# Kernel tuning notes

Measured on AMD Instinct MI355X. Metric: run time of the kernel, lower is better.

Reference implementation:

```python
import jax, jax.numpy as jnp
import numpy as np
from jax import lax

N_SAMPLES1 = 128   # self.n_samples[0]
K = 64             # k in sample_and_group
RADIUS = 0.4       # self.radius[0]
BN_EPS = 1e-5
NEG_INF = -1e8
DIMS0 = [6, 64, 64, 128]      # mlps_in[0][0] -> mlps[0]
DIMS1 = [131, 128, 128, 512]  # 128+3 -> mlps[1] (use_light_weight=False)


def _fps(pos, n):
    # pos: (N,3) -> (n,) indices; deterministic start at point 0
    Np = pos.shape[0]
    def body(carry, _):
        dists, last = carry
        d = jnp.sum((pos - pos[last]) ** 2, axis=-1)
        dists = jnp.minimum(dists, d)
        return (dists, jnp.argmax(dists).astype(jnp.int32)), last
    _, idxs = lax.scan(body, (jnp.full((Np,), 1e10, pos.dtype), jnp.int32(0)), None, length=n)
    return idxs


def _gather(values, idx):
    # values (B,N,C), idx (B,...) -> (B,...,C)
    return jax.vmap(lambda v, i: v[i])(values, idx)


def _conv_bn_relu(x, W, b, g, be):
    # 1x1 Conv2d + BatchNorm2d (training-mode batch stats) + ReLU; x (B,n,k,Cin)
    y = jnp.einsum('bnkc,cd->bnkd', x, W) + b
    m = jnp.mean(y, axis=(0, 1, 2), keepdims=True)
    v = jnp.mean(jnp.square(y - m), axis=(0, 1, 2), keepdims=True)
    return jax.nn.relu((y - m) * lax.rsqrt(v + BN_EPS) * g + be)


def _forward(x, pos,
             W00, b00, g00, be00, W01, b01, g01, be01, W02, b02, g02, be02,
             W10, b10, g10, be10, W11, b11, g11, be11, W12, b12, g12, be12):
    # ---- stage 0: FPS + kNN grouping + conv-MLP + radius-masked max pool ----
    fidx = jax.vmap(lambda p: _fps(p, N_SAMPLES1))(pos)          # (B,128)
    sp = _gather(pos, fidx)                                      # (B,128,3) sampled_pos
    # squared pairwise distances (||a||^2+||b||^2-2ab); topk/mask on sq dist is
    # equivalent to topk/mask on sqrt dist (monotone), avoids sqrt(0) NaN grads
    sq = (jnp.sum(sp ** 2, -1)[:, :, None] + jnp.sum(pos ** 2, -1)[:, None, :]
          - 2.0 * jnp.einsum('bmd,bnd->bmn', sp, pos))           # (B,128,N)
    sq = jnp.maximum(sq, 0.0)
    neg, tidx = lax.top_k(-sq, K)                                # smallest-k
    topk_sq = -neg                                               # (B,128,64)
    gp = _gather(pos, tidx) - sp[:, :, None, :]                  # centered grouped pos
    gf = jnp.concatenate([gp, _gather(x, tidx)], axis=-1)        # (B,128,64,6)
    for (W, b, g, be) in ((W00, b00, g00, be00), (W01, b01, g01, be01), (W02, b02, g02, be02)):
        gf = _conv_bn_relu(gf, W, b, g, be)                      # (B,128,64,128)
    mask = topk_sq <= RADIUS * RADIUS
    x1 = jnp.max(jnp.where(mask[..., None], gf, NEG_INF), axis=2)  # (B,128,128)
    # ---- stage 1: global (n_samples == 1) ----
    g2 = jnp.concatenate([sp, x1], axis=-1)[:, None]             # (B,1,128,131)
    for (W, b, g, be) in ((W10, b10, g10, be10), (W11, b11, g11, be11), (W12, b12, g12, be12)):
        g2 = _conv_bn_relu(g2, W, b, g, be)                      # (B,1,128,512)
    global_x = jnp.max(g2[:, 0], axis=1, keepdims=True)          # (B,1,512)
    return global_x


def setup_inputs() -> dict:
    key = jax.random.key(0)
    ks = jax.random.split(key, 16)
    B, N = 16, 8192
    inp = {
        'x': jax.random.normal(ks[0], (B, N, 3), jnp.float32),
        'pos': jax.random.uniform(ks[1], (B, N, 3), jnp.float32),
    }
    ki = 2
    for li, dims in enumerate([DIMS0, DIMS1]):
        for ci in range(3):
            cin, cout = dims[ci], dims[ci + 1]
            inp[f'W{li}{ci}'] = jax.random.normal(ks[ki], (cin, cout), jnp.float32) * 0.05
            inp[f'b{li}{ci}'] = jnp.zeros((cout,), jnp.float32)
            inp[f'g{li}{ci}'] = jnp.ones((cout,), jnp.float32)
            inp[f'be{li}{ci}'] = jnp.zeros((cout,), jnp.float32)
            ki += 1
    return inp


def reference(x, pos,
              W00, b00, g00, be00, W01, b01, g01, be01, W02, b02, g02, be02,
              W10, b10, g10, be10, W11, b11, g11, be11, W12, b12, g12, be12):
    global_x = _forward(x, pos,
                        W00, b00, g00, be00, W01, b01, g01, be01, W02, b02, g02, be02,
                        W10, b10, g10, be10, W11, b11, g11, be11, W12, b12, g12, be12)
    pos_out = jnp.zeros((pos.shape[0], 1, 3), pos.dtype)
    return global_x, pos_out
```

## Files before the change

### kernel.cpp

```cpp
#include <hip/hip_runtime.h>
#include <cstdint>
#include <cstddef>

#define NPTS 8192
#define BATCH 16
#define MS 128
#define KNB 64
#define NBLK (BATCH * MS)


__device__ __forceinline__ float dpp_wave_max_f32(float v) {
  v = fmaxf(v, __int_as_float(__builtin_amdgcn_update_dpp((int)0xff800000, __float_as_int(v), 0x111, 0xf, 0xf, false)));
  v = fmaxf(v, __int_as_float(__builtin_amdgcn_update_dpp((int)0xff800000, __float_as_int(v), 0x112, 0xf, 0xf, false)));
  v = fmaxf(v, __int_as_float(__builtin_amdgcn_update_dpp((int)0xff800000, __float_as_int(v), 0x114, 0xf, 0xf, false)));
  v = fmaxf(v, __int_as_float(__builtin_amdgcn_update_dpp((int)0xff800000, __float_as_int(v), 0x118, 0xf, 0xf, false)));
  v = fmaxf(v, __int_as_float(__builtin_amdgcn_update_dpp((int)0xff800000, __float_as_int(v), 0x142, 0xa, 0xf, false)));
  v = fmaxf(v, __int_as_float(__builtin_amdgcn_update_dpp((int)0xff800000, __float_as_int(v), 0x143, 0xc, 0xf, false)));
  return v;
}

__device__ __forceinline__ float dpp_wave_min_f32(float v) {
  v = fminf(v, __int_as_float(__builtin_amdgcn_update_dpp(0x7f800000, __float_as_int(v), 0x111, 0xf, 0xf, false)));
  v = fminf(v, __int_as_float(__builtin_amdgcn_update_dpp(0x7f800000, __float_as_int(v), 0x112, 0xf, 0xf, false)));
  v = fminf(v, __int_as_float(__builtin_amdgcn_update_dpp(0x7f800000, __float_as_int(v), 0x114, 0xf, 0xf, false)));
  v = fminf(v, __int_as_float(__builtin_amdgcn_update_dpp(0x7f800000, __float_as_int(v), 0x118, 0xf, 0xf, false)));
  v = fminf(v, __int_as_float(__builtin_amdgcn_update_dpp(0x7f800000, __float_as_int(v), 0x142, 0xa, 0xf, false)));
  v = fminf(v, __int_as_float(__builtin_amdgcn_update_dpp(0x7f800000, __float_as_int(v), 0x143, 0xc, 0xf, false)));
  return v;
}

__device__ __forceinline__ unsigned dpp_wave_min_u32(unsigned v) {
  unsigned o;
  o = (unsigned)__builtin_amdgcn_update_dpp((int)0xffffffffu, (int)v, 0x111, 0xf, 0xf, false); v = (o < v) ? o : v;
  o = (unsigned)__builtin_amdgcn_update_dpp((int)0xffffffffu, (int)v, 0x112, 0xf, 0xf, false); v = (o < v) ? o : v;
  o = (unsigned)__builtin_amdgcn_update_dpp((int)0xffffffffu, (int)v, 0x114, 0xf, 0xf, false); v = (o < v) ? o : v;
  o = (unsigned)__builtin_amdgcn_update_dpp((int)0xffffffffu, (int)v, 0x118, 0xf, 0xf, false); v = (o < v) ? o : v;
  o = (unsigned)__builtin_amdgcn_update_dpp((int)0xffffffffu, (int)v, 0x142, 0xa, 0xf, false); v = (o < v) ? o : v;
  o = (unsigned)__builtin_amdgcn_update_dpp((int)0xffffffffu, (int)v, 0x143, 0xc, 0xf, false); v = (o < v) ? o : v;
  return v;
}

__device__ __forceinline__ float dpp_row_max_f32(float v) {
  v = fmaxf(v, __int_as_float(__builtin_amdgcn_update_dpp((int)0xff800000, __float_as_int(v), 0x111, 0xf, 0xf, false)));
  v = fmaxf(v, __int_as_float(__builtin_amdgcn_update_dpp((int)0xff800000, __float_as_int(v), 0x112, 0xf, 0xf, false)));
  v = fmaxf(v, __int_as_float(__builtin_amdgcn_update_dpp((int)0xff800000, __float_as_int(v), 0x114, 0xf, 0xf, false)));
  v = fmaxf(v, __int_as_float(__builtin_amdgcn_update_dpp((int)0xff800000, __float_as_int(v), 0x118, 0xf, 0xf, false)));
  return v;
}

__device__ __forceinline__ unsigned dpp_row_min_u32(unsigned v) {
  unsigned o;
  o = (unsigned)__builtin_amdgcn_update_dpp((int)0xffffffffu, (int)v, 0x111, 0xf, 0xf, false); v = (o < v) ? o : v;
  o = (unsigned)__builtin_amdgcn_update_dpp((int)0xffffffffu, (int)v, 0x112, 0xf, 0xf, false); v = (o < v) ? o : v;
  o = (unsigned)__builtin_amdgcn_update_dpp((int)0xffffffffu, (int)v, 0x114, 0xf, 0xf, false); v = (o < v) ? o : v;
  o = (unsigned)__builtin_amdgcn_update_dpp((int)0xffffffffu, (int)v, 0x118, 0xf, 0xf, false); v = (o < v) ? o : v;
  return v;
}

__device__ __forceinline__ float dpp_quad_min_f32(float v) {
  v = fminf(v, __int_as_float(__builtin_amdgcn_update_dpp(0x7f800000, __float_as_int(v), 0x111, 0xf, 0xf, false)));
  v = fminf(v, __int_as_float(__builtin_amdgcn_update_dpp(0x7f800000, __float_as_int(v), 0x112, 0xf, 0xf, false)));
  return v;
}

__device__ __forceinline__ unsigned dpp_quad_min_u32(unsigned v) {
  unsigned o;
  o = (unsigned)__builtin_amdgcn_update_dpp((int)0xffffffffu, (int)v, 0x111, 0xf, 0xf, false); v = (o < v) ? o : v;
  o = (unsigned)__builtin_amdgcn_update_dpp((int)0xffffffffu, (int)v, 0x112, 0xf, 0xf, false); v = (o < v) ? o : v;
  return v;
}

#define FPS_STEP(J)                                                        \
  {                                                                        \
    const int i = J * 1024 + t;                                            \
    const float dx = px[i] - lx;                                           \
    const float dy = py[i] - ly;                                           \
    const float dz = pz[i] - lz;                                           \
    const float d = dx * dx + dy * dy + dz * dz;                           \
    md##J = fminf(md##J, d);                                               \
  }

#define FPS_RESCAN(J)                                                      \
  if (md##J == wv) best = (unsigned)(J * 1024 + t);

__global__ __launch_bounds__(1024, 4) void fps_kernel(const float* __restrict__ pos,
                                                      float* __restrict__ sp) {
#pragma clang fp contract(off)
  extern __shared__ float smem[];
  float* px = smem;
  float* py = smem + NPTS;
  float* pz = smem + 2 * NPTS;
  __shared__ float wval[2][16];
  __shared__ unsigned widx[2][16];
  const int b = blockIdx.x;
  const float* P = pos + (size_t)b * NPTS * 3;
  const int t = threadIdx.x;
  const int wave = t >> 6;
  const int lane = t & 63;
  float md0 = 1e10f, md1 = 1e10f, md2 = 1e10f, md3 = 1e10f;
  float md4 = 1e10f, md5 = 1e10f, md6 = 1e10f, md7 = 1e10f;
  for (int i = t; i < NPTS; i += 1024) {
    px[i] = P[i * 3 + 0];
    py[i] = P[i * 3 + 1];
    pz[i] = P[i * 3 + 2];
  }
  float lx = P[0], ly = P[1], lz = P[2];
  __syncthreads();
  for (int it = 0; it < MS; ++it) {
    if (t == 0) {
      sp[((size_t)b * MS + it) * 3 + 0] = lx;
      sp[((size_t)b * MS + it) * 3 + 1] = ly;
      sp[((size_t)b * MS + it) * 3 + 2] = lz;
    }
    FPS_STEP(0) FPS_STEP(1) FPS_STEP(2) FPS_STEP(3)
    FPS_STEP(4) FPS_STEP(5) FPS_STEP(6) FPS_STEP(7)
    const float m01 = fmaxf(md0, md1), m23 = fmaxf(md2, md3);
    const float m45 = fmaxf(md4, md5), m67 = fmaxf(md6, md7);
    const float bv = fmaxf(fmaxf(m01, m23), fmaxf(m45, m67));
    const float wv = __int_as_float(
        __builtin_amdgcn_readlane(__float_as_int(dpp_wave_max_f32(bv)), 63));
    unsigned best = 0xffffffffu;
    if (bv == wv) {
      FPS_RESCAN(7) FPS_RESCAN(6) FPS_RESCAN(5) FPS_RESCAN(4)
      FPS_RESCAN(3) FPS_RESCAN(2) FPS_RESCAN(1) FPS_RESCAN(0)
    }
    const unsigned wi =
        (unsigned)__builtin_amdgcn_readlane((int)dpp_wave_min_u32(best), 63);
    const int par = it & 1;
    if (lane == 0) { wval[par][wave] = wv; widx[par][wave] = wi; }
    __syncthreads();
    const float a = wval[par][lane & 15];
    const float M = __int_as_float(
        __builtin_amdgcn_readlane(__float_as_int(dpp_row_max_f32(a)), 15));
    const unsigned c2 = (a == M) ? widx[par][lane & 15] : 0xffffffffu;
    const unsigned idx =
        (unsigned)__builtin_amdgcn_readlane((int)dpp_row_min_u32(c2), 15);
    lx = px[idx];
    ly = py[idx];
    lz = pz[idx];
  }
}

__global__ __launch_bounds__(256) void knn_kernel(const float* __restrict__ pos,
                                                  const float* __restrict__ xf,
                                                  const float* __restrict__ sp,
                                                  float* __restrict__ gf0,
                                                  float* __restrict__ sqsel) {
#pragma clang fp contract(off)
  __shared__ float sqv[NPTS];
  __shared__ float wval[2][4];
  __shared__ unsigned widx[2][4];
  __shared__ int sel_i[KNB];
  __shared__ float sel_v[KNB];
  const int bm = blockIdx.x;
  const int b = bm >> 7;
  const float* P = pos + (size_t)b * NPTS * 3;
  const float sx = sp[bm * 3 + 0], sy = sp[bm * 3 + 1], sz = sp[bm * 3 + 2];
  const float nsp = sx * sx + sy * sy + sz * sz;
  const int t = threadIdx.x;
  const int wave = t >> 6;
  const int lane = t & 63;
  for (int j = 0; j < 32; ++j) {
    const int i = j * 256 + t;
    const float qx = P[i * 3 + 0], qy = P[i * 3 + 1], qz = P[i * 3 + 2];
    const float npos = qx * qx + qy * qy + qz * qz;
    const float dt = sx * qx + sy * qy + sz * qz;
    float sq = (nsp + npos) - 2.0f * dt;
    sq = fmaxf(sq, 0.0f);
    sqv[i] = sq;
  }
  __syncthreads();
  float cv;
  unsigned ci;
  {
    unsigned long long k0 = ~0ULL;
    for (int j = 0; j < 32; ++j) {
      const int i = j * 256 + t;
      const unsigned long long key =
          ((unsigned long long)__float_as_uint(sqv[i]) << 32) | (unsigned)i;
      if (key < k0) k0 = key;
    }
    cv = __uint_as_float((unsigned)(k0 >> 32));
    ci = (unsigned)k0;
  }
  for (int round = 0; round < KNB; ++round) {
    const float wv = __int_as_float(
        __builtin_amdgcn_readlane(__float_as_int(dpp_wave_min_f32(cv)), 63));
    const unsigned sel = (cv == wv) ? ci : 0xffffffffu;
    const unsigned wi =
        (unsigned)__builtin_amdgcn_readlane((int)dpp_wave_min_u32(sel), 63);
    const int par = round & 1;
    if (lane == 0) { wval[par][wave] = wv; widx[par][wave] = wi; }
    __syncthreads();
    const float a = wval[par][lane & 3];
    const float M = __int_as_float(
        __builtin_amdgcn_readlane(__float_as_int(dpp_quad_min_f32(a)), 3));
    const unsigned c2 = (a == M) ? widx[par][lane & 3] : 0xffffffffu;
    const unsigned idx =
        (unsigned)__builtin_amdgcn_readlane((int)dpp_quad_min_u32(c2), 3);
    const int col = (int)(idx & 255u);
    if (t == col) {
      sel_i[round] = (int)idx;
      sel_v[round] = M;
      sqv[idx] = __uint_as_float(0x7f800000u);
    }
    if (wave == (col >> 6)) {
      float v = __uint_as_float(0x7f800000u);
      unsigned ii = 0xffffffffu;
      if (lane < 32) {
        const int i = lane * 256 + col;
        v = sqv[i];
        if (i == (int)idx) v = __uint_as_float(0x7f800000u);
        ii = (unsigned)i;
      }
      const float mv = __int_as_float(
          __builtin_amdgcn_readlane(__float_as_int(dpp_wave_min_f32(v)), 63));
      const unsigned s2 = (v == mv) ? ii : 0xffffffffu;
      const unsigned mi =
          (unsigned)__builtin_amdgcn_readlane((int)dpp_wave_min_u32(s2), 63);
      if (t == col) { cv = mv; ci = mi; }
    }
  }
  __syncthreads();
  if (t < KNB) {
    const int i = sel_i[t];
    const float* X = xf + (size_t)b * NPTS * 3;
    const size_t base = ((size_t)bm * KNB + t) * 6;
    gf0[base + 0] = P[i * 3 + 0] - sx;
    gf0[base + 1] = P[i * 3 + 1] - sy;
    gf0[base + 2] = P[i * 3 + 2] - sz;
    gf0[base + 3] = X[i * 3 + 0];
    gf0[base + 4] = X[i * 3 + 1];
    gf0[base + 5] = X[i * 3 + 2];
    sqsel[(size_t)bm * KNB + t] = sel_v[t];
  }
}

template <int MODE>
__global__ __launch_bounds__(256) void chain_kernel(
    const float* __restrict__ gf0,
    const float* __restrict__ W0, const float* __restrict__ B0,
    const float* __restrict__ W1, const float* __restrict__ B1,
    const float* __restrict__ W2, const float* __restrict__ B2,
    const float* __restrict__ sc1, const float* __restrict__ sh1,
    const float* __restrict__ sc2, const float* __restrict__ sh2,
    const float* __restrict__ sc3, const float* __restrict__ sh3,
    const float* __restrict__ sqsel,
    float* __restrict__ psum, float* __restrict__ psq, float* __restrict__ x1,
    float* __restrict__ z2out) {
  __shared__ float tA[64 * 65];
  __shared__ float tB[64 * 65];
  __shared__ float wbuf[64 * 64];
  __shared__ float in6[64 * 8];
  __shared__ float sqs[64];
  const int blk = blockIdx.x;
  const int t = threadIdx.x;
  {
    const float* G = gf0 + (size_t)blk * 64 * 6;
    for (int i = t; i < 384; i += 256) in6[(i / 6) * 8 + (i % 6)] = G[i];
    for (int i = t; i < 384; i += 256) wbuf[i] = W0[i];
    if (MODE == 4 && t < 64) sqs[t] = sqsel[(size_t)blk * 64 + t];
  }
  __syncthreads();
  const int r = t >> 2;
  const int c0 = (t & 3) * 16;
  float acc[16];
#pragma unroll
  for (int j = 0; j < 16; ++j) acc[j] = B0[c0 + j];
  for (int cin = 0; cin < 6; ++cin) {
    const float a = in6[r * 8 + cin];
#pragma unroll
    for (int j = 0; j < 16; ++j) acc[j] = fmaf(a, wbuf[cin * 64 + c0 + j], acc[j]);
  }
  if (MODE == 1) {
#pragma unroll
    for (int j = 0; j < 16; ++j) tA[r * 65 + c0 + j] = acc[j];
    __syncthreads();
    if (t < 64) {
      float s = 0.f, q = 0.f;
      for (int r2 = 0; r2 < 64; ++r2) { const float v = tA[r2 * 65 + t]; s += v; q += v * v; }
      psum[(size_t)t * NBLK + blk] = s;
      psq[(size_t)t * NBLK + blk] = q;
    }
    return;
  }
#pragma unroll
  for (int j = 0; j < 16; ++j) {
    const int c = c0 + j;
    tA[r * 65 + c] = fmaxf(fmaf(acc[j], sc1[c], sh1[c]), 0.f);
  }
  __syncthreads();
  for (int i = t; i < 4096; i += 256) wbuf[i] = W1[i];
  __syncthreads();
#pragma unroll
  for (int j = 0; j < 16; ++j) acc[j] = B1[c0 + j];
  for (int cin = 0; cin < 64; ++cin) {
    const float a = tA[r * 65 + cin];
    const float4* w4 = reinterpret_cast<const float4*>(&wbuf[cin * 64 + c0]);
#pragma unroll
    for (int k = 0; k < 4; ++k) {
      const float4 w = w4[k];
      acc[k * 4 + 0] = fmaf(a, w.x, acc[k * 4 + 0]);
      acc[k * 4 + 1] = fmaf(a, w.y, acc[k * 4 + 1]);
      acc[k * 4 + 2] = fmaf(a, w.z, acc[k * 4 + 2]);
      acc[k * 4 + 3] = fmaf(a, w.w, acc[k * 4 + 3]);
    }
  }
  if (MODE == 2) {
#pragma unroll
    for (int j = 0; j < 16; ++j) tB[r * 65 + c0 + j] = acc[j];
    __syncthreads();
    if (t < 64) {
      float s = 0.f, q = 0.f;
      for (int r2 = 0; r2 < 64; ++r2) { const float v = tB[r2 * 65 + t]; s += v; q += v * v; }
      psum[(size_t)t * NBLK + blk] = s;
      psq[(size_t)t * NBLK + blk] = q;
    }
    return;
  }
#pragma unroll
  for (int j = 0; j < 16; ++j) {
    const int c = c0 + j;
    tB[r * 65 + c] = fmaxf(fmaf(acc[j], sc2[c], sh2[c]), 0.f);
  }
  for (int hc = 0; hc < 2; ++hc) {
    __syncthreads();
    for (int i = t; i < 4096; i += 256) {
      const int cin = i >> 6, cc = i & 63;
      wbuf[i] = W2[cin * 128 + hc * 64 + cc];
    }
    if (MODE == 3 && hc == 0 && z2out != nullptr) {
      float* Zg = z2out + (size_t)blk * 4096;
      for (int i = t; i < 4096; i += 256) Zg[i] = tB[(i >> 6) * 65 + (i & 63)];
    }
    __syncthreads();
    float st_s = 0.f, st_q = 0.f, mx = -1e8f;
    for (int rh = 0; rh < 2; ++rh) {
      const int rr = rh * 32 + (t >> 3);
      const int cc0 = (t & 7) * 8;
      float a3[8];
#pragma unroll
      for (int j = 0; j < 8; ++j) a3[j] = B2[hc * 64 + cc0 + j];
      for (int cin = 0; cin < 64; ++cin) {
        const float a = tB[rr * 65 + cin];
        const float4* w4 = reinterpret_cast<const float4*>(&wbuf[cin * 64 + cc0]);
#pragma unroll
        for (int k = 0; k < 2; ++k) {
          const float4 w = w4[k];
          a3[k * 4 + 0] = fmaf(a, w.x, a3[k * 4 + 0]);
          a3[k * 4 + 1] = fmaf(a, w.y, a3[k * 4 + 1]);
          a3[k * 4 + 2] = fmaf(a, w.z, a3[k * 4 + 2]);
          a3[k * 4 + 3] = fmaf(a, w.w, a3[k * 4 + 3]);
        }
      }
      __syncthreads();
#pragma unroll
      for (int j = 0; j < 8; ++j) tA[(t >> 3) * 65 + cc0 + j] = a3[j];
      __syncthreads();
      if (t < 64) {
        if (MODE == 3) {
          for (int q2 = 0; q2 < 32; ++q2) { const float v = tA[q2 * 65 + t]; st_s += v; st_q += v * v; }
        } else {
          const float scv = sc3[hc * 64 + t], shv = sh3[hc * 64 + t];
          for (int q2 = 0; q2 < 32; ++q2) {
            const int kidx = rh * 32 + q2;
            const float y = tA[q2 * 65 + t];
            const float act = fmaxf(fmaf(y, scv, shv), 0.f);
            const float v = (sqs[kidx] <= 0.16f) ? act : -1e8f;
            mx = fmaxf(mx, v);
          }
        }
      }
      __syncthreads();
    }
    if (t < 64) {
      if (MODE == 3) {
        psum[(size_t)(hc * 64 + t) * NBLK + blk] = st_s;
        psq[(size_t)(hc * 64 + t) * NBLK + blk] = st_q;
      } else if (MODE == 4) {
        x1[(size_t)blk * 128 + hc * 64 + t] = mx;
      }
    }
  }
}

__global__ __launch_bounds__(256) void chain4c_kernel(
    const float* __restrict__ z2, const float* __restrict__ W2, const float* __restrict__ B2,
    const float* __restrict__ sc3, const float* __restrict__ sh3,
    const float* __restrict__ sqsel, float* __restrict__ x1) {
  __shared__ float tA[64 * 65];
  __shared__ float tB[64 * 65];
  __shared__ float wbuf[64 * 64];
  __shared__ float sqs[64];
  const int blk = blockIdx.x;
  const int t = threadIdx.x;
  const float* Zg = z2 + (size_t)blk * 4096;
  for (int i = t; i < 4096; i += 256) tB[(i >> 6) * 65 + (i & 63)] = Zg[i];
  if (t < 64) sqs[t] = sqsel[(size_t)blk * 64 + t];
  for (int hc = 0; hc < 2; ++hc) {
    __syncthreads();
    for (int i = t; i < 4096; i += 256) {
      const int cin = i >> 6, cc = i & 63;
      wbuf[i] = W2[cin * 128 + hc * 64 + cc];
    }
    __syncthreads();
    float mx = -1e8f;
    for (int rh = 0; rh < 2; ++rh) {
      const int rr = rh * 32 + (t >> 3);
      const int cc0 = (t & 7) * 8;
      float a3[8];
#pragma unroll
      for (int j = 0; j < 8; ++j) a3[j] = B2[hc * 64 + cc0 + j];
      for (int cin = 0; cin < 64; ++cin) {
        const float a = tB[rr * 65 + cin];
        const float4* w4 = reinterpret_cast<const float4*>(&wbuf[cin * 64 + cc0]);
#pragma unroll
        for (int k = 0; k < 2; ++k) {
          const float4 w = w4[k];
          a3[k * 4 + 0] = fmaf(a, w.x, a3[k * 4 + 0]);
          a3[k * 4 + 1] = fmaf(a, w.y, a3[k * 4 + 1]);
          a3[k * 4 + 2] = fmaf(a, w.z, a3[k * 4 + 2]);
          a3[k * 4 + 3] = fmaf(a, w.w, a3[k * 4 + 3]);
        }
      }
      __syncthreads();
#pragma unroll
      for (int j = 0; j < 8; ++j) tA[(t >> 3) * 65 + cc0 + j] = a3[j];
      __syncthreads();
      if (t < 64) {
        const float scv = sc3[hc * 64 + t], shv = sh3[hc * 64 + t];
        for (int q2 = 0; q2 < 32; ++q2) {
          const int kidx = rh * 32 + q2;
          const float y = tA[q2 * 65 + t];
          const float act = fmaxf(fmaf(y, scv, shv), 0.f);
          const float v = (sqs[kidx] <= 0.16f) ? act : -1e8f;
          mx = fmaxf(mx, v);
        }
      }
      __syncthreads();
    }
    if (t < 64) x1[(size_t)blk * 128 + hc * 64 + t] = mx;
  }
}

__global__ __launch_bounds__(256) void p_stats(const float* __restrict__ psum,
                                               const float* __restrict__ psq,
                                               float invN,
                                               const float* __restrict__ g,
                                               const float* __restrict__ be,
                                               float* __restrict__ sc,
                                               float* __restrict__ sh) {
  const int c = blockIdx.x;
  const int t = threadIdx.x;
  double s = 0.0, q = 0.0;
  for (int k = t; k < NBLK; k += 256) {
    s += (double)psum[(size_t)c * NBLK + k];
    q += (double)psq[(size_t)c * NBLK + k];
  }
  __shared__ double ss[256], qq[256];
  ss[t] = s;
  qq[t] = q;
  __syncthreads();
  for (int st = 128; st > 0; st >>= 1) {
    if (t < st) { ss[t] += ss[t + st]; qq[t] += qq[t + st]; }
    __syncthreads();
  }
  if (t == 0) {
    const double mean = ss[0] * (double)invN;
    double var = qq[0] * (double)invN - mean * mean;
    if (var < 0.0) var = 0.0;
    const float scl = (float)((double)g[c] / sqrt(var + 1e-5));
    sc[c] = scl;
    sh[c] = be[c] - (float)mean * scl;
  }
}

__global__ __launch_bounds__(128) void s1_kernel(const float* __restrict__ sp,
                                                 const float* __restrict__ x1,
                                                 const float* __restrict__ W,
                                                 const float* __restrict__ bia,
                                                 float* __restrict__ y1) {
  __shared__ float row[132];
  const int rowid = blockIdx.x;
  const int t = threadIdx.x;
  if (t < 3) row[t] = sp[(size_t)rowid * 3 + t];
  row[3 + t] = x1[(size_t)rowid * 128 + t];
  __syncthreads();
  float acc = bia[t];
  for (int cin = 0; cin < 131; ++cin) acc = fmaf(row[cin], W[(size_t)cin * 128 + t], acc);
  y1[(size_t)rowid * 128 + t] = acc;
}

__global__ __launch_bounds__(128) void s2_kernel(const float* __restrict__ y1,
                                                 const float* __restrict__ sc, const float* __restrict__ sh,
                                                 const float* __restrict__ W, const float* __restrict__ bia,
                                                 float* __restrict__ y2) {
  __shared__ float row[128];
  const int rowid = blockIdx.x;
  const int t = threadIdx.x;
  row[t] = fmaxf(fmaf(y1[(size_t)rowid * 128 + t], sc[t], sh[t]), 0.f);
  __syncthreads();
  float acc = bia[t];
  for (int cin = 0; cin < 128; ++cin) acc = fmaf(row[cin], W[(size_t)cin * 128 + t], acc);
  y2[(size_t)rowid * 128 + t] = acc;
}

__global__ __launch_bounds__(256) void s3_kernel(const float* __restrict__ y2,
                                                 const float* __restrict__ sc, const float* __restrict__ sh,
                                                 const float* __restrict__ W, const float* __restrict__ bia,
                                                 float* __restrict__ y3) {
  __shared__ float row[128];
  const int rowid = blockIdx.x;
  const int t = threadIdx.x;
  if (t < 128) row[t] = fmaxf(fmaf(y2[(size_t)rowid * 128 + t], sc[t], sh[t]), 0.f);
  __syncthreads();
  for (int h = 0; h < 2; ++h) {
    const int c = h * 256 + t;
    float acc = bia[c];
    for (int cin = 0; cin < 128; ++cin) acc = fmaf(row[cin], W[(size_t)cin * 512 + c], acc);
    y3[(size_t)rowid * 512 + c] = acc;
  }
}

__global__ __launch_bounds__(256) void s_stats(const float* __restrict__ y, int C, int rows,
                                               const float* __restrict__ g, const float* __restrict__ be,
                                               float* __restrict__ sc, float* __restrict__ sh) {
  const int c = blockIdx.x;
  const int t = threadIdx.x;
  double s = 0.0, q = 0.0;
  for (int r2 = t; r2 < rows; r2 += 256) {
    const double v = (double)y[(size_t)r2 * C + c];
    s += v;
    q += v * v;
  }
  __shared__ double ss[256], qq[256];
  ss[t] = s;
  qq[t] = q;
  __syncthreads();
  for (int st = 128; st > 0; st >>= 1) {
    if (t < st) { ss[t] += ss[t + st]; qq[t] += qq[t + st]; }
    __syncthreads();
  }
  if (t == 0) {
    const double mean = ss[0] / rows;
    double var = qq[0] / rows - mean * mean;
    if (var < 0.0) var = 0.0;
    const float scl = (float)((double)g[c] / sqrt(var + 1e-5));
    sc[c] = scl;
    sh[c] = be[c] - (float)mean * scl;
  }
}

__global__ __launch_bounds__(256) void final_kernel(const float* __restrict__ y3,
                                                    const float* __restrict__ sc, const float* __restrict__ sh,
                                                    float* __restrict__ out) {
  const int gid = blockIdx.x * 256 + threadIdx.x;
  const int b = gid >> 9;
  const int c = gid & 511;
  const float scv = sc[c], shv = sh[c];
  float mx = -3.402823466e+38f;
  for (int m = 0; m < 128; ++m) {
    const float v = fmaxf(fmaf(y3[((size_t)(b * 128 + m)) * 512 + c], scv, shv), 0.f);
    mx = fmaxf(mx, v);
  }
  out[gid] = mx;
  if (gid < 48) out[8192 + gid] = 0.f;
}

extern "C" void kernel_launch(void* const* d_in, const int* in_sizes, int n_in,
                              void* d_out, int out_size, void* d_ws, size_t ws_size,
                              hipStream_t stream) {
  const float* x    = (const float*)d_in[0];
  const float* pos  = (const float*)d_in[1];
  const float* W00  = (const float*)d_in[2];
  const float* b00  = (const float*)d_in[3];
  const float* g00  = (const float*)d_in[4];
  const float* be00 = (const float*)d_in[5];
  const float* W01  = (const float*)d_in[6];
  const float* b01  = (const float*)d_in[7];
  const float* g01  = (const float*)d_in[8];
  const float* be01 = (const float*)d_in[9];
  const float* W02  = (const float*)d_in[10];
  const float* b02  = (const float*)d_in[11];
  const float* g02  = (const float*)d_in[12];
  const float* be02 = (const float*)d_in[13];
  const float* W10  = (const float*)d_in[14];
  const float* b10  = (const float*)d_in[15];
  const float* g10  = (const float*)d_in[16];
  const float* be10 = (const float*)d_in[17];
  const float* W11  = (const float*)d_in[18];
  const float* b11  = (const float*)d_in[19];
  const float* g11  = (const float*)d_in[20];
  const float* be11 = (const float*)d_in[21];
  const float* W12  = (const float*)d_in[22];
  const float* b12  = (const float*)d_in[23];
  const float* g12  = (const float*)d_in[24];
  const float* be12 = (const float*)d_in[25];

  float* w = (float*)d_ws;
  float* sp    = w;
  float* gf0   = sp + 6144;
  float* sqsel = gf0 + 786432;
  float* x1    = sqsel + 131072;
  float* parts = x1 + 262144;
  float* psum  = parts;
  float* psq   = parts + 128 * NBLK;
  float* st    = parts + 524288;
  float* sc1 = st + 0,    *sh1 = st + 64;
  float* sc2 = st + 128,  *sh2 = st + 192;
  float* sc3 = st + 256,  *sh3 = st + 384;
  float* t1sc = st + 512, *t1sh = st + 640;
  float* t2sc = st + 768, *t2sh = st + 896;
  float* t3sc = st + 1024, *t3sh = st + 1536;
  float* y1s = st + 2048;
  float* y2s = y1s + 262144;
  float* y3s = y2s + 262144;
  const size_t Z2OFF = 3284992;
  const size_t Z2LEN = (size_t)NBLK * 4096;
  const bool cache_ok = ws_size >= (Z2OFF + Z2LEN) * sizeof(float);
  float* z2 = cache_ok ? (w + Z2OFF) : nullptr;

  fps_kernel<<<BATCH, 1024, 3 * NPTS * sizeof(float), stream>>>(pos, sp);
  knn_kernel<<<BATCH * MS, 256, 0, stream>>>(pos, x, sp, gf0, sqsel);

  const float invN0 = 1.0f / (float)(NBLK * KNB);
  chain_kernel<1><<<NBLK, 256, 0, stream>>>(gf0, W00, b00, W01, b01, W02, b02,
                                            sc1, sh1, sc2, sh2, sc3, sh3, sqsel, psum, psq, x1, nullptr);
  p_stats<<<64, 256, 0, stream>>>(psum, psq, invN0, g00, be00, sc1, sh1);
  chain_kernel<2><<<NBLK, 256, 0, stream>>>(gf0, W00, b00, W01, b01, W02, b02,
                                            sc1, sh1, sc2, sh2, sc3, sh3, sqsel, psum, psq, x1, nullptr);
  p_stats<<<64, 256, 0, stream>>>(psum, psq, invN0, g01, be01, sc2, sh2);
  chain_kernel<3><<<NBLK, 256, 0, stream>>>(gf0, W00, b00, W01, b01, W02, b02,
                                            sc1, sh1, sc2, sh2, sc3, sh3, sqsel, psum, psq, x1, z2);
  p_stats<<<128, 256, 0, stream>>>(psum, psq, invN0, g02, be02, sc3, sh3);
  if (cache_ok) {
    chain4c_kernel<<<NBLK, 256, 0, stream>>>(z2, W02, b02, sc3, sh3, sqsel, x1);
  } else {
    chain_kernel<4><<<NBLK, 256, 0, stream>>>(gf0, W00, b00, W01, b01, W02, b02,
                                              sc1, sh1, sc2, sh2, sc3, sh3, sqsel, psum, psq, x1, nullptr);
  }

  s1_kernel<<<NBLK, 128, 0, stream>>>(sp, x1, W10, b10, y1s);
  s_stats<<<128, 256, 0, stream>>>(y1s, 128, NBLK, g10, be10, t1sc, t1sh);
  s2_kernel<<<NBLK, 128, 0, stream>>>(y1s, t1sc, t1sh, W11, b11, y2s);
  s_stats<<<128, 256, 0, stream>>>(y2s, 128, NBLK, g11, be11, t2sc, t2sh);
  s3_kernel<<<NBLK, 256, 0, stream>>>(y2s, t2sc, t2sh, W12, b12, y3s);
  s_stats<<<512, 256, 0, stream>>>(y3s, 512, NBLK, g12, be12, t3sc, t3sh);
  final_kernel<<<32, 256, 0, stream>>>(y3s, t3sc, t3sh, (float*)d_out);
}
```

Before: 519.6 us.

## Materialize stage-0 MLP pre-activations per layer instead of recomputing chain

Replaces the recompute-the-whole-chain approach (each BN pass re-running all earlier layers) with per-layer kernels that store pre-activation outputs to workspace and reload them for the next layer. Layer 2/3 GEMMs use a 4x4 register tile with float4 shared-memory loads, and the final masked max pool becomes a light streaming kernel. This trades redundant FLOPs for extra global-memory traffic (about 32M floats written and read back) and needs a much larger workspace. It falls back to the old chain path when the workspace is too small.

After: 443.2 us. 14.7% less time.

```diff
diff --git a/kernel.cpp b/kernel.cpp
--- a/kernel.cpp
+++ b/kernel.cpp
@@ -7,7 +7,6 @@
 #define MS 128
 #define KNB 64
 #define NBLK (BATCH * MS)
-
 
 __device__ __forceinline__ float dpp_wave_max_f32(float v) {
   v = fmaxf(v, __int_as_float(__builtin_amdgcn_update_dpp((int)0xff800000, __float_as_int(v), 0x111, 0xf, 0xf, false)));
@@ -236,6 +235,191 @@
   }
 }
 
+
+__global__ __launch_bounds__(256) void l1_kernel(
+    const float* __restrict__ gf0, const float* __restrict__ W0,
+    const float* __restrict__ B0,
+    float* __restrict__ psum, float* __restrict__ psq,
+    float* __restrict__ y1pre) {
+  __shared__ float in6[64 * 8];
+  __shared__ float wbuf[384];
+  __shared__ float out[64 * 65];
+  const int blk = blockIdx.x;
+  const int t = threadIdx.x;
+  const float* G = gf0 + (size_t)blk * 384;
+  for (int i = t; i < 384; i += 256) in6[(i / 6) * 8 + (i % 6)] = G[i];
+  for (int i = t; i < 384; i += 256) wbuf[i] = W0[i];
+  __syncthreads();
+  const int r = t >> 2;
+  const int c0 = (t & 3) * 16;
+  float acc[16];
+#pragma unroll
+  for (int j = 0; j < 16; ++j) acc[j] = B0[c0 + j];
+  for (int cin = 0; cin < 6; ++cin) {
+    const float a = in6[r * 8 + cin];
+#pragma unroll
+    for (int j = 0; j < 16; ++j) acc[j] = fmaf(a, wbuf[cin * 64 + c0 + j], acc[j]);
+  }
+#pragma unroll
+  for (int j = 0; j < 16; ++j) out[r * 65 + c0 + j] = acc[j];
+  __syncthreads();
+  if (t < 64) {
+    float s = 0.f, q = 0.f;
+    for (int r2 = 0; r2 < 64; ++r2) { const float v = out[r2 * 65 + t]; s += v; q += v * v; }
+    psum[(size_t)t * NBLK + blk] = s;
+    psq[(size_t)t * NBLK + blk] = q;
+  }
+  float* Y = y1pre + (size_t)blk * 4096;
+  for (int i = t; i < 4096; i += 256) Y[i] = out[(i >> 6) * 65 + (i & 63)];
+}
+
+__global__ __launch_bounds__(256) void l2_kernel(
+    const float* __restrict__ ypre, const float* __restrict__ sc,
+    const float* __restrict__ sh, const float* __restrict__ W1,
+    const float* __restrict__ B1,
+    float* __restrict__ psum, float* __restrict__ psq,
+    float* __restrict__ yout) {
+  __shared__ float As[64 * 68];
+  __shared__ float Bs[64 * 64];
+  __shared__ float out[64 * 68];
+  const int blk = blockIdx.x;
+  const int t = threadIdx.x;
+  const float* Y = ypre + (size_t)blk * 4096;
+  for (int i = t; i < 4096; i += 256) {
+    const int c = i & 63;
+    As[(i >> 6) * 68 + c] = fmaxf(fmaf(Y[i], sc[c], sh[c]), 0.f);
+  }
+  for (int i = t; i < 4096; i += 256) Bs[i] = W1[i];
+  __syncthreads();
+  const int tr = t >> 4;
+  const int tc4 = (t & 15) * 4;
+  float acc[4][4];
+#pragma unroll
+  for (int s = 0; s < 4; ++s)
+#pragma unroll
+    for (int j = 0; j < 4; ++j) acc[s][j] = B1[tc4 + j];
+  for (int k0 = 0; k0 < 64; k0 += 4) {
+    float4 av[4];
+#pragma unroll
+    for (int s = 0; s < 4; ++s)
+      av[s] = *reinterpret_cast<const float4*>(&As[(tr + 16 * s) * 68 + k0]);
+#pragma unroll
+    for (int kk = 0; kk < 4; ++kk) {
+      const float4 bv = *reinterpret_cast<const float4*>(&Bs[(k0 + kk) * 64 + tc4]);
+#pragma unroll
+      for (int s = 0; s < 4; ++s) {
+        const float a = (kk == 0) ? av[s].x : (kk == 1) ? av[s].y
+                       : (kk == 2) ? av[s].z : av[s].w;
+        acc[s][0] = fmaf(a, bv.x, acc[s][0]);
+        acc[s][1] = fmaf(a, bv.y, acc[s][1]);
+        acc[s][2] = fmaf(a, bv.z, acc[s][2]);
+        acc[s][3] = fmaf(a, bv.w, acc[s][3]);
+      }
+    }
+  }
+#pragma unroll
+  for (int s = 0; s < 4; ++s) {
+    float4 o;
+    o.x = acc[s][0]; o.y = acc[s][1]; o.z = acc[s][2]; o.w = acc[s][3];
+    *reinterpret_cast<float4*>(&out[(tr + 16 * s) * 68 + tc4]) = o;
+  }
+  __syncthreads();
+  if (t < 64) {
+    float s = 0.f, q = 0.f;
+    for (int r2 = 0; r2 < 64; ++r2) { const float v = out[r2 * 68 + t]; s += v; q += v * v; }
+    psum[(size_t)t * NBLK + blk] = s;
+    psq[(size_t)t * NBLK + blk] = q;
+  }
+  float* O = yout + (size_t)blk * 4096;
+  for (int i = t; i < 4096; i += 256) O[i] = out[(i >> 6) * 68 + (i & 63)];
+}
+
+__global__ __launch_bounds__(256) void l3_kernel(
+    const float* __restrict__ ypre, const float* __restrict__ sc,
+    const float* __restrict__ sh, const float* __restrict__ W2,
+    const float* __restrict__ B2,
+    float* __restrict__ psum, float* __restrict__ psq,
+    float* __restrict__ yout) {
+  __shared__ float As[64 * 68];
+  __shared__ float Bs[64 * 64];
+  __shared__ float out[64 * 68];
+  const int blk = blockIdx.x;
+  const int t = threadIdx.x;
+  const float* Y = ypre + (size_t)blk * 4096;
+  for (int i = t; i < 4096; i += 256) {
+    const int c = i & 63;
+    As[(i >> 6) * 68 + c] = fmaxf(fmaf(Y[i], sc[c], sh[c]), 0.f);
+  }
+  const int tr = t >> 4;
+  const int tc4 = (t & 15) * 4;
+  for (int hc = 0; hc < 2; ++hc) {
+    __syncthreads();
+    for (int i = t; i < 4096; i += 256)
+      Bs[i] = W2[(i >> 6) * 128 + hc * 64 + (i & 63)];
+    __syncthreads();
+    float acc[4][4];
+#pragma unroll
+    for (int s = 0; s < 4; ++s)
+#pragma unroll
+      for (int j = 0; j < 4; ++j) acc[s][j] = B2[hc * 64 + tc4 + j];
+    for (int k0 = 0; k0 < 64; k0 += 4) {
+      float4 av[4];
+#pragma unroll
+      for (int s = 0; s < 4; ++s)
+        av[s] = *reinterpret_cast<const float4*>(&As[(tr + 16 * s) * 68 + k0]);
+#pragma unroll
+      for (int kk = 0; kk < 4; ++kk) {
+        const float4 bv = *reinterpret_cast<const float4*>(&Bs[(k0 + kk) * 64 + tc4]);
+#pragma unroll
+        for (int s = 0; s < 4; ++s) {
+          const float a = (kk == 0) ? av[s].x : (kk == 1) ? av[s].y
+                         : (kk == 2) ? av[s].z : av[s].w;
+          acc[s][0] = fmaf(a, bv.x, acc[s][0]);
+          acc[s][1] = fmaf(a, bv.y, acc[s][1]);
+          acc[s][2] = fmaf(a, bv.z, acc[s][2]);
+          acc[s][3] = fmaf(a, bv.w, acc[s][3]);
+        }
+      }
+    }
+#pragma unroll
+    for (int s = 0; s < 4; ++s) {
+      float4 o;
+      o.x = acc[s][0]; o.y = acc[s][1]; o.z = acc[s][2]; o.w = acc[s][3];
+      *reinterpret_cast<float4*>(&out[(tr + 16 * s) * 68 + tc4]) = o;
+    }
+    __syncthreads();
+    if (t < 64) {
+      float s = 0.f, q = 0.f;
+      for (int r2 = 0; r2 < 64; ++r2) { const float v = out[r2 * 68 + t]; s += v; q += v * v; }
+      psum[(size_t)(hc * 64 + t) * NBLK + blk] = s;
+      psq[(size_t)(hc * 64 + t) * NBLK + blk] = q;
+    }
+    float* O = yout + (size_t)blk * 8192;
+    for (int i = t; i < 4096; i += 256)
+      O[(i >> 6) * 128 + hc * 64 + (i & 63)] = out[(i >> 6) * 68 + (i & 63)];
+  }
+}
+
+__global__ __launch_bounds__(128) void l4_kernel(
+    const float* __restrict__ y3pre, const float* __restrict__ sc3,
+    const float* __restrict__ sh3, const float* __restrict__ sqsel,
+    float* __restrict__ x1) {
+  __shared__ float sqs[64];
+  const int blk = blockIdx.x;
+  const int t = threadIdx.x;
+  if (t < 64) sqs[t] = sqsel[(size_t)blk * 64 + t];
+  __syncthreads();
+  const float scv = sc3[t], shv = sh3[t];
+  const float* Y = y3pre + (size_t)blk * 8192;
+  float mx = -1e8f;
+  for (int r = 0; r < 64; ++r) {
+    const float act = fmaxf(fmaf(Y[r * 128 + t], scv, shv), 0.f);
+    const float v = (sqs[r] <= 0.16f) ? act : -1e8f;
+    mx = fmaxf(mx, v);
+  }
+  x1[(size_t)blk * 128 + t] = mx;
+}
+
 template <int MODE>
 __global__ __launch_bounds__(256) void chain_kernel(
     const float* __restrict__ gf0,
@@ -246,8 +430,7 @@
     const float* __restrict__ sc2, const float* __restrict__ sh2,
     const float* __restrict__ sc3, const float* __restrict__ sh3,
     const float* __restrict__ sqsel,
-    float* __restrict__ psum, float* __restrict__ psq, float* __restrict__ x1,
-    float* __restrict__ z2out) {
+    float* __restrict__ psum, float* __restrict__ psq, float* __restrict__ x1) {
   __shared__ float tA[64 * 65];
   __shared__ float tB[64 * 65];
   __shared__ float wbuf[64 * 64];
@@ -328,10 +511,6 @@
     for (int i = t; i < 4096; i += 256) {
       const int cin = i >> 6, cc = i & 63;
       wbuf[i] = W2[cin * 128 + hc * 64 + cc];
-    }
-    if (MODE == 3 && hc == 0 && z2out != nullptr) {
-      float* Zg = z2out + (size_t)blk * 4096;
-      for (int i = t; i < 4096; i += 256) Zg[i] = tB[(i >> 6) * 65 + (i & 63)];
     }
     __syncthreads();
     float st_s = 0.f, st_q = 0.f, mx = -1e8f;
@@ -381,65 +560,6 @@
         x1[(size_t)blk * 128 + hc * 64 + t] = mx;
       }
     }
-  }
-}
-
-__global__ __launch_bounds__(256) void chain4c_kernel(
-    const float* __restrict__ z2, const float* __restrict__ W2, const float* __restrict__ B2,
-    const float* __restrict__ sc3, const float* __restrict__ sh3,
-    const float* __restrict__ sqsel, float* __restrict__ x1) {
-  __shared__ float tA[64 * 65];
-  __shared__ float tB[64 * 65];
-  __shared__ float wbuf[64 * 64];
-  __shared__ float sqs[64];
-  const int blk = blockIdx.x;
-  const int t = threadIdx.x;
-  const float* Zg = z2 + (size_t)blk * 4096;
-  for (int i = t; i < 4096; i += 256) tB[(i >> 6) * 65 + (i & 63)] = Zg[i];
-  if (t < 64) sqs[t] = sqsel[(size_t)blk * 64 + t];
-  for (int hc = 0; hc < 2; ++hc) {
-    __syncthreads();
-    for (int i = t; i < 4096; i += 256) {
-      const int cin = i >> 6, cc = i & 63;
-      wbuf[i] = W2[cin * 128 + hc * 64 + cc];
-    }
-    __syncthreads();
-    float mx = -1e8f;
-    for (int rh = 0; rh < 2; ++rh) {
-      const int rr = rh * 32 + (t >> 3);
-      const int cc0 = (t & 7) * 8;
-      float a3[8];
-#pragma unroll
-      for (int j = 0; j < 8; ++j) a3[j] = B2[hc * 64 + cc0 + j];
-      for (int cin = 0; cin < 64; ++cin) {
-        const float a = tB[rr * 65 + cin];
-        const float4* w4 = reinterpret_cast<const float4*>(&wbuf[cin * 64 + cc0]);
-#pragma unroll
-        for (int k = 0; k < 2; ++k) {
-          const float4 w = w4[k];
-          a3[k * 4 + 0] = fmaf(a, w.x, a3[k * 4 + 0]);
-          a3[k * 4 + 1] = fmaf(a, w.y, a3[k * 4 + 1]);
-          a3[k * 4 + 2] = fmaf(a, w.z, a3[k * 4 + 2]);
-          a3[k * 4 + 3] = fmaf(a, w.w, a3[k * 4 + 3]);
-        }
-      }
-      __syncthreads();
-#pragma unroll
-      for (int j = 0; j < 8; ++j) tA[(t >> 3) * 65 + cc0 + j] = a3[j];
-      __syncthreads();
-      if (t < 64) {
-        const float scv = sc3[hc * 64 + t], shv = sh3[hc * 64 + t];
-        for (int q2 = 0; q2 < 32; ++q2) {
-          const int kidx = rh * 32 + q2;
-          const float y = tA[q2 * 65 + t];
-          const float act = fmaxf(fmaf(y, scv, shv), 0.f);
-          const float v = (sqs[kidx] <= 0.16f) ? act : -1e8f;
-          mx = fmaxf(mx, v);
-        }
-      }
-      __syncthreads();
-    }
-    if (t < 64) x1[(size_t)blk * 128 + hc * 64 + t] = mx;
   }
 }
 
@@ -615,29 +735,37 @@
   float* y1s = st + 2048;
   float* y2s = y1s + 262144;
   float* y3s = y2s + 262144;
-  const size_t Z2OFF = 3284992;
-  const size_t Z2LEN = (size_t)NBLK * 4096;
-  const bool cache_ok = ws_size >= (Z2OFF + Z2LEN) * sizeof(float);
-  float* z2 = cache_ok ? (w + Z2OFF) : nullptr;
+  const size_t BASE = 3284992;
+  float* y1pre = w + BASE;
+  float* y2pre = y1pre + 8388608;
+  float* y3pre = y2pre + 8388608;
+  const size_t NEED = BASE + 8388608ULL * 2 + 16777216ULL;
+  const bool big = ws_size >= NEED * sizeof(float);
 
   fps_kernel<<<BATCH, 1024, 3 * NPTS * sizeof(float), stream>>>(pos, sp);
   knn_kernel<<<BATCH * MS, 256, 0, stream>>>(pos, x, sp, gf0, sqsel);
 
   const float invN0 = 1.0f / (float)(NBLK * KNB);
-  chain_kernel<1><<<NBLK, 256, 0, stream>>>(gf0, W00, b00, W01, b01, W02, b02,
-                                            sc1, sh1, sc2, sh2, sc3, sh3, sqsel, psum, psq, x1, nullptr);
-  p_stats<<<64, 256, 0, stream>>>(psum, psq, invN0, g00, be00, sc1, sh1);
-  chain_kernel<2><<<NBLK, 256, 0, stream>>>(gf0, W00, b00, W01, b01, W02, b02,
-                                            sc1, sh1, sc2, sh2, sc3, sh3, sqsel, psum, psq, x1, nullptr);
-  p_stats<<<64, 256, 0, stream>>>(psum, psq, invN0, g01, be01, sc2, sh2);
-  chain_kernel<3><<<NBLK, 256, 0, stream>>>(gf0, W00, b00, W01, b01, W02, b02,
-                                            sc1, sh1, sc2, sh2, sc3, sh3, sqsel, psum, psq, x1, z2);
-  p_stats<<<128, 256, 0, stream>>>(psum, psq, invN0, g02, be02, sc3, sh3);
-  if (cache_ok) {
-    chain4c_kernel<<<NBLK, 256, 0, stream>>>(z2, W02, b02, sc3, sh3, sqsel, x1);
+  if (big) {
+    l1_kernel<<<NBLK, 256, 0, stream>>>(gf0, W00, b00, psum, psq, y1pre);
+    p_stats<<<64, 256, 0, stream>>>(psum, psq, invN0, g00, be00, sc1, sh1);
+    l2_kernel<<<NBLK, 256, 0, stream>>>(y1pre, sc1, sh1, W01, b01, psum, psq, y2pre);
+    p_stats<<<64, 256, 0, stream>>>(psum, psq, invN0, g01, be01, sc2, sh2);
+    l3_kernel<<<NBLK, 256, 0, stream>>>(y2pre, sc2, sh2, W02, b02, psum, psq, y3pre);
+    p_stats<<<128, 256, 0, stream>>>(psum, psq, invN0, g02, be02, sc3, sh3);
+    l4_kernel<<<NBLK, 128, 0, stream>>>(y3pre, sc3, sh3, sqsel, x1);
   } else {
+    chain_kernel<1><<<NBLK, 256, 0, stream>>>(gf0, W00, b00, W01, b01, W02, b02,
+                                              sc1, sh1, sc2, sh2, sc3, sh3, sqsel, psum, psq, x1);
+    p_stats<<<64, 256, 0, stream>>>(psum, psq, invN0, g00, be00, sc1, sh1);
+    chain_kernel<2><<<NBLK, 256, 0, stream>>>(gf0, W00, b00, W01, b01, W02, b02,
+                                              sc1, sh1, sc2, sh2, sc3, sh3, sqsel, psum, psq, x1);
+    p_stats<<<64, 256, 0, stream>>>(psum, psq, invN0, g01, be01, sc2, sh2);
+    chain_kernel<3><<<NBLK, 256, 0, stream>>>(gf0, W00, b00, W01, b01, W02, b02,
+                                              sc1, sh1, sc2, sh2, sc3, sh3, sqsel, psum, psq, x1);
+    p_stats<<<128, 256, 0, stream>>>(psum, psq, invN0, g02, be02, sc3, sh3);
     chain_kernel<4><<<NBLK, 256, 0, stream>>>(gf0, W00, b00, W01, b01, W02, b02,
-                                              sc1, sh1, sc2, sh2, sc3, sh3, sqsel, psum, psq, x1, nullptr);
+                                              sc1, sh1, sc2, sh2, sc3, sh3, sqsel, psum, psq, x1);
   }
 
   s1_kernel<<<NBLK, 128, 0, stream>>>(sp, x1, W10, b10, y1s);
```
